# Performance work log

Hardware: AMD Instinct MI355X
Metric: run time of the kernel (lower is better)

## Reference

```python
import jax, jax.numpy as jnp
import numpy as np

L = 3; D = 128; H = 8; RBF = 16; SBF = 112
N = 60000; E = 300000; A = 8000; G = 256
EPS = 1e-8


def setup_inputs() -> dict:
    key = jax.random.key(0)
    ks = jax.random.split(key, 32)
    p = lambda i, shape: jax.random.normal(ks[i], shape, jnp.float32) * 0.05
    inp = {}
    inp['x'] = jax.random.normal(ks[0], (N, D), jnp.float32)
    inp['node_rbf'] = jax.random.uniform(ks[1], (N, RBF), jnp.float32)
    inp['edge_sbf'] = jax.random.uniform(ks[2], (E, SBF), jnp.float32)
    inp['edge_index'] = jax.random.randint(ks[3], (2, E), 0, N)
    inp['pair_atom_idx'] = jax.random.randint(ks[4], (E,), 0, A)
    inp['edge_index_0'] = jax.random.randint(ks[5], (N,), 0, A)
    inp['atom_batch'] = jnp.sort(jax.random.randint(ks[6], (A,), 0, G))
    inp['batch'] = jnp.sort(jax.random.randint(ks[7], (N,), 0, G))
    inp['edgenn_w1'] = p(8, (L, D, D)); inp['edgenn_b1'] = jnp.zeros((L, D))
    inp['edgenn_w2'] = p(9, (L, D, D)); inp['edgenn_b2'] = jnp.zeros((L, D))
    inp['conv_wq'] = p(10, (L, D, D)); inp['conv_wk'] = p(11, (L, D, D))
    inp['conv_wv'] = p(12, (L, D, D)); inp['conv_we'] = p(13, (L, D, D))
    inp['conv_wsbf'] = p(14, (L, SBF, D)); inp['conv_bsbf'] = jnp.zeros((L, D))
    inp['conv_wrbf'] = p(15, (L, RBF, D))
    inp['dense_w'] = p(16, (L, D, D)); inp['dense_b'] = jnp.zeros((L, D))
    inp['bf_w'] = p(17, (L, 2, D, D)); inp['bf_b'] = jnp.zeros((L, 2, D))
    inp['af_w'] = p(18, (L, 4, D, D)); inp['af_b'] = jnp.zeros((L, 4, D))
    inp['read_wrbf'] = p(19, (L + 1, RBF, D))
    inp['read_w1'] = p(20, (L + 1, D, D)); inp['read_b1'] = jnp.zeros((L + 1, D))
    inp['read_w2'] = p(21, (L + 1, D, D)); inp['read_b2'] = jnp.zeros((L + 1, D))
    inp['read_w3'] = p(22, (L + 1, D, 1)); inp['read_b3'] = jnp.zeros((L + 1, 1))
    return inp


def _forward(x, node_rbf, edge_sbf, edge_index, pair_atom_idx, edge_index_0,
             atom_batch, batch, edgenn_w1, edgenn_b1, edgenn_w2, edgenn_b2,
             conv_wq, conv_wk, conv_wv, conv_we, conv_wsbf, conv_bsbf, conv_wrbf,
             dense_w, dense_b, bf_w, bf_b, af_w, af_b,
             read_wrbf, read_w1, read_b1, read_w2, read_b2, read_w3, read_b3):
    segsum = jax.ops.segment_sum
    silu = jax.nn.silu
    src, dst = edge_index[0], edge_index[1]
    C = D // H

    def readout(i, h):
        # AtomWise: rbf-gated node features, scatter to atoms, small MLP -> [A,1]
        g = h * (node_rbf @ read_wrbf[i])
        atoms = segsum(g, edge_index_0, num_segments=A)
        a = silu(atoms @ read_w1[i] + read_b1[i])
        a = silu(a @ read_w2[i] + read_b2[i])
        return a @ read_w3[i] + read_b3[i]

    def res_block(h, w, b):
        # DimeNet-style ResidualLayer: x + act(lin2(act(lin1(x))))
        return h + silu(silu(h @ w[0] + b[0]) @ w[1] + b[1])

    def graph_norm(h):
        # batch-aware LayerNorm (graph mode, affine=False)
        cnt = segsum(jnp.ones((N,), h.dtype), batch, num_segments=G) * D
        mean = segsum(h.sum(-1), batch, num_segments=G) / cnt
        hc = h - mean[batch][:, None]
        var = segsum((hc * hc).sum(-1), batch, num_segments=G) / cnt
        return hc * jax.lax.rsqrt(var + EPS)[batch][:, None]

    out = x
    results = readout(0, out)
    for i in range(L):
        res0 = out
        atoms_rep = segsum(out, edge_index_0, num_segments=A)  # scatter_add to atoms
        ea = atoms_rep[pair_atom_idx]                           # gather per conv-edge
        ea = silu(ea @ edgenn_w1[i] + edgenn_b1[i]) @ edgenn_w2[i] + edgenn_b2[i]
        # SBFTransformerConv: TransformerConv with sbf-modulated messages + rbf gate
        q = (out @ conv_wq[i]).reshape(N, H, C)
        k = (out @ conv_wk[i]).reshape(N, H, C)
        v = (out @ conv_wv[i]).reshape(N, H, C)
        ek = (ea @ conv_we[i]).reshape(E, H, C)
        kj = k[src] + ek
        logit = (q[dst] * kj).sum(-1) / jnp.sqrt(jnp.asarray(C, out.dtype))  # [E,H]
        m = jax.ops.segment_max(logit, dst, num_segments=N)
        ex = jnp.exp(logit - m[dst])
        alpha = ex / (segsum(ex, dst, num_segments=N)[dst] + 1e-16)
        sw = (edge_sbf @ conv_wsbf[i] + conv_bsbf[i]).reshape(E, H, C)
        msg = (v[src] + ek) * alpha[:, :, None] * sw
        h = segsum(msg, dst, num_segments=N).reshape(N, D)
        out = h * (node_rbf @ conv_wrbf[i])
        out = graph_norm(out)
        out = res_block(out, bf_w[i], bf_b[i])
        out = silu(out @ dense_w[i] + dense_b[i])
        out = out + res0
        out = res_block(out, af_w[i, :2], af_b[i, :2])
        out = res_block(out, af_w[i, 2:], af_b[i, 2:])
        results = results + readout(i + 1, out)
    graphs = segsum(results, atom_batch, num_segments=G)  # [G,1]
    return graphs.reshape(-1) / L


def reference(x, node_rbf, edge_sbf, edge_index, pair_atom_idx, edge_index_0,
              atom_batch, batch, edgenn_w1, edgenn_b1, edgenn_w2, edgenn_b2,
              conv_wq, conv_wk, conv_wv, conv_we, conv_wsbf, conv_bsbf, conv_wrbf,
              dense_w, dense_b, bf_w, bf_b, af_w, af_b,
              read_wrbf, read_w1, read_b1, read_w2, read_b2, read_w3, read_b3):
    return _forward(x, node_rbf, edge_sbf, edge_index, pair_atom_idx, edge_index_0,
                    atom_batch, batch, edgenn_w1, edgenn_b1, edgenn_w2, edgenn_b2,
                    conv_wq, conv_wk, conv_wv, conv_we, conv_wsbf, conv_bsbf, conv_wrbf,
                    dense_w, dense_b, bf_w, bf_b, af_w, af_b,
                    read_wrbf, read_w1, read_b1, read_w2, read_b2, read_w3, read_b3)
```

## Files before the change

### kernel.cpp

```cpp
#include <hip/hip_runtime.h>
#include <math.h>

#define D    128
#define NH   8
#define RBFD 16
#define SBFD 112
#define LAYERS 3

typedef __attribute__((ext_vector_type(8))) short bf16x8;
typedef __attribute__((ext_vector_type(4))) float f32x4;

__device__ __forceinline__ float siluf(float x){ return x / (1.0f + __expf(-x)); }

__device__ __forceinline__ short f2bf(float f){
  union { float f; unsigned u; } v; v.f = f;
  unsigned r = v.u + 0x7FFFu + ((v.u >> 16) & 1u);
  return (short)(r >> 16);
}
__device__ __forceinline__ float bflo(unsigned u){ return __uint_as_float(u << 16); }
__device__ __forceinline__ float bfhi(unsigned u){ return __uint_as_float(u & 0xFFFF0000u); }

template<int DIN, int ACT, bool GATHER, bool HASB, bool HASRES, bool PERM, bool OUTBF>
__global__ __launch_bounds__(256, 2) void k_gemm(
    const float* __restrict__ X, const int* __restrict__ gidx,
    const float* __restrict__ W, const float* __restrict__ bias,
    const float* res, void* __restrict__ Yv, const int* __restrict__ operm, int M)
{
  __shared__ short Wt[128 * 128];
  if (DIN < 128){
    for (int i = threadIdx.x; i < 128 * 128; i += 256) Wt[i] = 0;
    __syncthreads();
  }
  for (int i = threadIdx.x; i < DIN * 128; i += 256){
    int k = i >> 7, c = i & 127;
    Wt[c * 128 + k] = f2bf(W[i]);
  }
  __syncthreads();

  const int lane = threadIdx.x & 63;
  const int wave = threadIdx.x >> 6;
  const int col0 = lane & 15;
  const int kg   = lane >> 4;

  bf16x8 Bf[8][4];
  #pragma unroll
  for (int ct = 0; ct < 8; ct++)
    #pragma unroll
    for (int s = 0; s < 4; s++)
      Bf[ct][s] = *(const bf16x8*)&Wt[(ct * 16 + col0) * 128 + s * 32 + kg * 8];

  float bs[8];
  if (HASB){
    #pragma unroll
    for (int ct = 0; ct < 8; ct++) bs[ct] = bias[ct * 16 + col0];
  }

  float* __restrict__ Yf = (float*)Yv;
  unsigned short* __restrict__ Yb = (unsigned short*)Yv;

  const long tiles = ((long)M + 63) >> 6;
  for (long t = blockIdx.x; t < tiles; t += gridDim.x){
    const long rbase = t * 64 + wave * 16;
    const long arow  = rbase + col0;
    long srow = 0;
    if (arow < M) srow = GATHER ? (long)gidx[arow] : arow;
    const float* Xp = X + srow * DIN;

    bf16x8 Af[4];
    #pragma unroll
    for (int s = 0; s < 4; s++){
      const int kb = s * 32 + kg * 8;
      bf16x8 a;
      if (DIN == 128 || kb + 8 <= DIN){
        float4 lo = *(const float4*)(Xp + kb);
        float4 hi = *(const float4*)(Xp + kb + 4);
        a[0]=f2bf(lo.x); a[1]=f2bf(lo.y); a[2]=f2bf(lo.z); a[3]=f2bf(lo.w);
        a[4]=f2bf(hi.x); a[5]=f2bf(hi.y); a[6]=f2bf(hi.z); a[7]=f2bf(hi.w);
      } else {
        #pragma unroll
        for (int j = 0; j < 8; j++) a[j] = 0;
      }
      Af[s] = a;
    }

    f32x4 acc[8];
    #pragma unroll
    for (int ct = 0; ct < 8; ct++){ acc[ct][0]=0.f; acc[ct][1]=0.f; acc[ct][2]=0.f; acc[ct][3]=0.f; }
    #pragma unroll
    for (int ct = 0; ct < 8; ct++)
      #pragma unroll
      for (int s = 0; s < 4; s++)
        acc[ct] = __builtin_amdgcn_mfma_f32_16x16x32_bf16(Af[s], Bf[ct][s], acc[ct], 0, 0, 0);

    #pragma unroll
    for (int r = 0; r < 4; r++){
      const long orow = rbase + kg * 4 + r;
      if (orow >= M) continue;
      const long wrow = PERM ? (long)operm[orow] : orow;
      #pragma unroll
      for (int ct = 0; ct < 8; ct++){
        const int c = ct * 16 + col0;
        float v = acc[ct][r];
        if (HASB) v += bs[ct];
        if (ACT)  v = siluf(v);
        if (HASRES) v += res[orow * D + c];
        if (OUTBF) Yb[wrow * D + c] = (unsigned short)f2bf(v);
        else       Yf[wrow * D + c] = v;
      }
    }
  }
}

__global__ __launch_bounds__(256, 2) void k_gemm2(
    const float* __restrict__ X, const int* __restrict__ gidx,
    const float* __restrict__ W1, const float* __restrict__ b1,
    const float* __restrict__ W2, const float* __restrict__ b2,
    unsigned short* __restrict__ Y, const int* __restrict__ operm, int M)
{
  __shared__ short W1t[128 * 128];
  __shared__ short W2t[128 * 128];
  __shared__ short Ts[64 * 128];
  for (int i = threadIdx.x; i < 128 * 128; i += 256){
    int k = i >> 7, c = i & 127;
    W1t[c * 128 + k] = f2bf(W1[i]);
    W2t[c * 128 + k] = f2bf(W2[i]);
  }
  __syncthreads();

  const int lane = threadIdx.x & 63;
  const int wave = threadIdx.x >> 6;
  const int col0 = lane & 15;
  const int kg   = lane >> 4;

  bf16x8 B1f[8][4];
  #pragma unroll
  for (int ct = 0; ct < 8; ct++)
    #pragma unroll
    for (int s = 0; s < 4; s++)
      B1f[ct][s] = *(const bf16x8*)&W1t[(ct * 16 + col0) * 128 + s * 32 + kg * 8];

  float bs1[8], bs2[8];
  #pragma unroll
  for (int ct = 0; ct < 8; ct++){ bs1[ct] = b1[ct * 16 + col0]; bs2[ct] = b2[ct * 16 + col0]; }

  const long tiles = ((long)M + 63) >> 6;
  for (long t = blockIdx.x; t < tiles; t += gridDim.x){
    const long rbase = t * 64 + wave * 16;
    const long arow  = rbase + col0;
    long srow = 0;
    if (arow < M) srow = (long)gidx[arow];
    const float* Xp = X + srow * D;

    bf16x8 Af[4];
    #pragma unroll
    for (int s = 0; s < 4; s++){
      const int kb = s * 32 + kg * 8;
      float4 lo = *(const float4*)(Xp + kb);
      float4 hi = *(const float4*)(Xp + kb + 4);
      bf16x8 a;
      a[0]=f2bf(lo.x); a[1]=f2bf(lo.y); a[2]=f2bf(lo.z); a[3]=f2bf(lo.w);
      a[4]=f2bf(hi.x); a[5]=f2bf(hi.y); a[6]=f2bf(hi.z); a[7]=f2bf(hi.w);
      Af[s] = a;
    }

    f32x4 acc[8];
    #pragma unroll
    for (int ct = 0; ct < 8; ct++){ acc[ct][0]=0.f; acc[ct][1]=0.f; acc[ct][2]=0.f; acc[ct][3]=0.f; }
    #pragma unroll
    for (int ct = 0; ct < 8; ct++)
      #pragma unroll
      for (int s = 0; s < 4; s++)
        acc[ct] = __builtin_amdgcn_mfma_f32_16x16x32_bf16(Af[s], B1f[ct][s], acc[ct], 0, 0, 0);

    #pragma unroll
    for (int ct = 0; ct < 8; ct++){
      const int c = ct * 16 + col0;
      #pragma unroll
      for (int r = 0; r < 4; r++){
        const int row = wave * 16 + kg * 4 + r;
        const int gg = (c >> 3) ^ (row & 7);
        Ts[row * 128 + gg * 8 + (c & 7)] = f2bf(siluf(acc[ct][r] + bs1[ct]));
      }
    }
    __syncthreads();

    const int row2 = wave * 16 + col0;
    bf16x8 A2f[4];
    #pragma unroll
    for (int s = 0; s < 4; s++){
      const int chunk = (s * 4 + kg) ^ (row2 & 7);
      A2f[s] = *(const bf16x8*)&Ts[row2 * 128 + chunk * 8];
    }
    __syncthreads();

    #pragma unroll
    for (int ct = 0; ct < 8; ct++){ acc[ct][0]=0.f; acc[ct][1]=0.f; acc[ct][2]=0.f; acc[ct][3]=0.f; }
    #pragma unroll
    for (int ct = 0; ct < 8; ct++){
      bf16x8 B2v[4];
      #pragma unroll
      for (int s = 0; s < 4; s++)
        B2v[s] = *(const bf16x8*)&W2t[(ct * 16 + col0) * 128 + s * 32 + kg * 8];
      #pragma unroll
      for (int s = 0; s < 4; s++)
        acc[ct] = __builtin_amdgcn_mfma_f32_16x16x32_bf16(A2f[s], B2v[s], acc[ct], 0, 0, 0);
    }

    #pragma unroll
    for (int r = 0; r < 4; r++){
      const long orow = rbase + kg * 4 + r;
      if (orow >= M) continue;
      const long wrow = (long)operm[orow];
      #pragma unroll
      for (int ct = 0; ct < 8; ct++){
        const int c = ct * 16 + col0;
        Y[wrow * D + c] = (unsigned short)f2bf(acc[ct][r] + bs2[ct]);
      }
    }
  }
}

template<bool NORM>
__global__ __launch_bounds__(256, 2) void k_res2(
    const float* __restrict__ X,
    const float* __restrict__ W1, const float* __restrict__ b1,
    const float* __restrict__ W2, const float* __restrict__ b2,
    const int* __restrict__ batch, const float* __restrict__ meanG,
    const float* __restrict__ rstdG, float* __restrict__ Y, int M)
{
  __shared__ short W1t[128 * 128];
  __shared__ short W2t[128 * 128];
  __shared__ short Ts[64 * 128];
  for (int i = threadIdx.x; i < 128 * 128; i += 256){
    int k = i >> 7, c = i & 127;
    W1t[c * 128 + k] = f2bf(W1[i]);
    W2t[c * 128 + k] = f2bf(W2[i]);
  }
  __syncthreads();

  const int lane = threadIdx.x & 63;
  const int wave = threadIdx.x >> 6;
  const int col0 = lane & 15;
  const int kg   = lane >> 4;

  bf16x8 B1f[8][4];
  #pragma unroll
  for (int ct = 0; ct < 8; ct++)
    #pragma unroll
    for (int s = 0; s < 4; s++)
      B1f[ct][s] = *(const bf16x8*)&W1t[(ct * 16 + col0) * 128 + s * 32 + kg * 8];

  float bs1[8], bs2[8];
  #pragma unroll
  for (int ct = 0; ct < 8; ct++){ bs1[ct] = b1[ct * 16 + col0]; bs2[ct] = b2[ct * 16 + col0]; }

  const long tiles = ((long)M + 63) >> 6;
  for (long t = blockIdx.x; t < tiles; t += gridDim.x){
    const long rbase = t * 64 + wave * 16;
    const long arow  = rbase + col0;
    const float* Xp = X + (arow < M ? arow : 0) * D;
    float xm = 0.f, xr = 1.f;
    if (NORM && arow < M){ int g = batch[arow]; xm = meanG[g]; xr = rstdG[g]; }

    bf16x8 Af[4];
    #pragma unroll
    for (int s = 0; s < 4; s++){
      const int kb = s * 32 + kg * 8;
      float4 lo = *(const float4*)(Xp + kb);
      float4 hi = *(const float4*)(Xp + kb + 4);
      bf16x8 a;
      a[0]=f2bf((lo.x-xm)*xr); a[1]=f2bf((lo.y-xm)*xr); a[2]=f2bf((lo.z-xm)*xr); a[3]=f2bf((lo.w-xm)*xr);
      a[4]=f2bf((hi.x-xm)*xr); a[5]=f2bf((hi.y-xm)*xr); a[6]=f2bf((hi.z-xm)*xr); a[7]=f2bf((hi.w-xm)*xr);
      Af[s] = a;
    }

    f32x4 acc[8];
    #pragma unroll
    for (int ct = 0; ct < 8; ct++){ acc[ct][0]=0.f; acc[ct][1]=0.f; acc[ct][2]=0.f; acc[ct][3]=0.f; }
    #pragma unroll
    for (int ct = 0; ct < 8; ct++)
      #pragma unroll
      for (int s = 0; s < 4; s++)
        acc[ct] = __builtin_amdgcn_mfma_f32_16x16x32_bf16(Af[s], B1f[ct][s], acc[ct], 0, 0, 0);

    #pragma unroll
    for (int ct = 0; ct < 8; ct++){
      const int c = ct * 16 + col0;
      #pragma unroll
      for (int r = 0; r < 4; r++){
        const int row = wave * 16 + kg * 4 + r;
        const int gg = (c >> 3) ^ (row & 7);
        Ts[row * 128 + gg * 8 + (c & 7)] = f2bf(siluf(acc[ct][r] + bs1[ct]));
      }
    }
    __syncthreads();

    const int row2 = wave * 16 + col0;
    bf16x8 A2f[4];
    #pragma unroll
    for (int s = 0; s < 4; s++){
      const int chunk = (s * 4 + kg) ^ (row2 & 7);
      A2f[s] = *(const bf16x8*)&Ts[row2 * 128 + chunk * 8];
    }
    __syncthreads();

    #pragma unroll
    for (int ct = 0; ct < 8; ct++){ acc[ct][0]=0.f; acc[ct][1]=0.f; acc[ct][2]=0.f; acc[ct][3]=0.f; }
    #pragma unroll
    for (int ct = 0; ct < 8; ct++){
      bf16x8 B2v[4];
      #pragma unroll
      for (int s = 0; s < 4; s++)
        B2v[s] = *(const bf16x8*)&W2t[(ct * 16 + col0) * 128 + s * 32 + kg * 8];
      #pragma unroll
      for (int s = 0; s < 4; s++)
        acc[ct] = __builtin_amdgcn_mfma_f32_16x16x32_bf16(A2f[s], B2v[s], acc[ct], 0, 0, 0);
    }

    #pragma unroll
    for (int r = 0; r < 4; r++){
      const long orow = rbase + kg * 4 + r;
      if (orow >= M) continue;
      float rm = 0.f, rr = 1.f;
      if (NORM){ int g = batch[orow]; rm = meanG[g]; rr = rstdG[g]; }
      #pragma unroll
      for (int ct = 0; ct < 8; ct++){
        const int c = ct * 16 + col0;
        float base = X[orow * D + c];
        if (NORM) base = (base - rm) * rr;
        Y[orow * D + c] = base + siluf(acc[ct][r] + bs2[ct]);
      }
    }
  }
}

__global__ __launch_bounds__(256, 2) void k_read2(
    const float* __restrict__ X,
    const float* __restrict__ W1, const float* __restrict__ b1,
    const float* __restrict__ W2, const float* __restrict__ b2,
    const float* __restrict__ w3, const float* __restrict__ b3,
    float* __restrict__ results, int M)
{
  __shared__ short W1t[128 * 128];
  __shared__ short W2t[128 * 128];
  __shared__ short Ts[64 * 128];
  for (int i = threadIdx.x; i < 128 * 128; i += 256){
    int k = i >> 7, c = i & 127;
    W1t[c * 128 + k] = f2bf(W1[i]);
    W2t[c * 128 + k] = f2bf(W2[i]);
  }
  __syncthreads();

  const int lane = threadIdx.x & 63;
  const int wave = threadIdx.x >> 6;
  const int col0 = lane & 15;
  const int kg   = lane >> 4;

  bf16x8 B1f[8][4];
  #pragma unroll
  for (int ct = 0; ct < 8; ct++)
    #pragma unroll
    for (int s = 0; s < 4; s++)
      B1f[ct][s] = *(const bf16x8*)&W1t[(ct * 16 + col0) * 128 + s * 32 + kg * 8];

  float bs1[8], bs2[8], w3v[8];
  #pragma unroll
  for (int ct = 0; ct < 8; ct++){
    bs1[ct] = b1[ct * 16 + col0];
    bs2[ct] = b2[ct * 16 + col0];
    w3v[ct] = w3[ct * 16 + col0];
  }
  const float b3v = b3[0];

  const long tiles = ((long)M + 63) >> 6;
  for (long t = blockIdx.x; t < tiles; t += gridDim.x){
    const long rbase = t * 64 + wave * 16;
    const long arow  = rbase + col0;
    const float* Xp = X + (arow < M ? arow : 0) * D;

    bf16x8 Af[4];
    #pragma unroll
    for (int s = 0; s < 4; s++){
      const int kb = s * 32 + kg * 8;
      float4 lo = *(const float4*)(Xp + kb);
      float4 hi = *(const float4*)(Xp + kb + 4);
      bf16x8 a;
      a[0]=f2bf(lo.x); a[1]=f2bf(lo.y); a[2]=f2bf(lo.z); a[3]=f2bf(lo.w);
      a[4]=f2bf(hi.x); a[5]=f2bf(hi.y); a[6]=f2bf(hi.z); a[7]=f2bf(hi.w);
      Af[s] = a;
    }

    f32x4 acc[8];
    #pragma unroll
    for (int ct = 0; ct < 8; ct++){ acc[ct][0]=0.f; acc[ct][1]=0.f; acc[ct][2]=0.f; acc[ct][3]=0.f; }
    #pragma unroll
    for (int ct = 0; ct < 8; ct++)
      #pragma unroll
      for (int s = 0; s < 4; s++)
        acc[ct] = __builtin_amdgcn_mfma_f32_16x16x32_bf16(Af[s], B1f[ct][s], acc[ct], 0, 0, 0);

    #pragma unroll
    for (int ct = 0; ct < 8; ct++){
      const int c = ct * 16 + col0;
      #pragma unroll
      for (int r = 0; r < 4; r++){
        const int row = wave * 16 + kg * 4 + r;
        const int gg = (c >> 3) ^ (row & 7);
        Ts[row * 128 + gg * 8 + (c & 7)] = f2bf(siluf(acc[ct][r] + bs1[ct]));
      }
    }
    __syncthreads();

    const int row2 = wave * 16 + col0;
    bf16x8 A2f[4];
    #pragma unroll
    for (int s = 0; s < 4; s++){
      const int chunk = (s * 4 + kg) ^ (row2 & 7);
      A2f[s] = *(const bf16x8*)&Ts[row2 * 128 + chunk * 8];
    }
    __syncthreads();

    #pragma unroll
    for (int ct = 0; ct < 8; ct++){ acc[ct][0]=0.f; acc[ct][1]=0.f; acc[ct][2]=0.f; acc[ct][3]=0.f; }
    #pragma unroll
    for (int ct = 0; ct < 8; ct++){
      bf16x8 B2v[4];
      #pragma unroll
      for (int s = 0; s < 4; s++)
        B2v[s] = *(const bf16x8*)&W2t[(ct * 16 + col0) * 128 + s * 32 + kg * 8];
      #pragma unroll
      for (int s = 0; s < 4; s++)
        acc[ct] = __builtin_amdgcn_mfma_f32_16x16x32_bf16(A2f[s], B2v[s], acc[ct], 0, 0, 0);
    }

    #pragma unroll
    for (int r = 0; r < 4; r++){
      float vr = 0.f;
      #pragma unroll
      for (int ct = 0; ct < 8; ct++)
        vr += siluf(acc[ct][r] + bs2[ct]) * w3v[ct];
      #pragma unroll
      for (int off = 1; off < 16; off <<= 1) vr += __shfl_xor(vr, off, 64);
      const long orow = rbase + kg * 4 + r;
      if (col0 == 0 && orow < M) results[orow] += vr + b3v;
    }
  }
}

__global__ void k_hist(const int* __restrict__ idx, int* __restrict__ cnt, int M)
{
  for (long i = (long)blockIdx.x * 256 + threadIdx.x; i < M; i += (long)gridDim.x * 256)
    atomicAdd(&cnt[idx[i]], 1);
}

__global__ void k_scan(const int* __restrict__ cnt, int* __restrict__ rowptr, int M)
{
  __shared__ int buf[1024];
  const int tid = threadIdx.x;
  const int PT = 16;
  int carry = 0;
  for (int base = 0; base < M; base += 1024 * PT){
    int loc[PT]; int s = 0;
    #pragma unroll
    for (int j = 0; j < PT; j++){
      int i = base + tid * PT + j;
      loc[j] = (i < M) ? cnt[i] : 0;
      s += loc[j];
    }
    buf[tid] = s; __syncthreads();
    for (int off = 1; off < 1024; off <<= 1){
      int t = (tid >= off) ? buf[tid - off] : 0;
      __syncthreads();
      buf[tid] += t;
      __syncthreads();
    }
    int run = buf[tid] - s + carry;
    carry += buf[1023];
    __syncthreads();
    #pragma unroll
    for (int j = 0; j < PT; j++){
      int i = base + tid * PT + j;
      if (i < M) rowptr[i] = run;
      run += loc[j];
    }
  }
  if (tid == 0) rowptr[M] = carry;
}

__global__ void k_fill(const int* __restrict__ idx, const int* __restrict__ rowptr,
                       int* __restrict__ cursor, int* __restrict__ ids, int M)
{
  for (long i = (long)blockIdx.x * 256 + threadIdx.x; i < M; i += (long)gridDim.x * 256){
    int sgm = idx[i];
    int pos = atomicAdd(&cursor[sgm], 1);
    ids[rowptr[sgm] + pos] = (int)i;
  }
}

__global__ void k_invsrc(const int* __restrict__ eids, const int* __restrict__ srcA,
                         int* __restrict__ invD, int* __restrict__ srcCSR, int E_)
{
  for (long i = (long)blockIdx.x * 256 + threadIdx.x; i < E_; i += (long)gridDim.x * 256){
    int e = eids[i];
    invD[e] = (int)i;
    srcCSR[i] = srcA[e];
  }
}

__global__ __launch_bounds__(256) void k_gather_sum(
    const float* __restrict__ X, const int* __restrict__ rowptr,
    const int* __restrict__ ids, float* __restrict__ Yat, int A_)
{
  const int lane = threadIdx.x & 63;
  const int wv   = threadIdx.x >> 6;
  for (long a = (long)blockIdx.x * 4 + wv; a < A_; a += (long)gridDim.x * 4){
    int beg = rowptr[a], end = rowptr[a + 1];
    float a0 = 0.f, a1 = 0.f;
    for (int i = beg; i < end; i++){
      const float* xp = X + (long)ids[i] * D;
      a0 += xp[lane]; a1 += xp[lane + 64];
    }
    Yat[a * D + lane] = a0; Yat[a * D + lane + 64] = a1;
  }
}

__global__ __launch_bounds__(256) void k_gather_gate_sum(
    const float* __restrict__ X, const float* __restrict__ rbf,
    const float* __restrict__ Wr, const int* __restrict__ rowptr,
    const int* __restrict__ ids, float* __restrict__ Yat, int A_)
{
  __shared__ float Wrs[RBFD * D];
  for (int i = threadIdx.x; i < RBFD * D; i += 256) Wrs[i] = Wr[i];
  __syncthreads();
  const int lane = threadIdx.x & 63;
  const int wv   = threadIdx.x >> 6;
  for (long a = (long)blockIdx.x * 4 + wv; a < A_; a += (long)gridDim.x * 4){
    int beg = rowptr[a], end = rowptr[a + 1];
    float a0 = 0.f, a1 = 0.f;
    for (int i = beg; i < end; i++){
      long n = ids[i];
      const float* xp = X + n * D;
      const float* rb = rbf + n * RBFD;
      float g0 = 0.f, g1 = 0.f;
      #pragma unroll
      for (int r = 0; r < RBFD; r++){
        float rv = rb[r];
        g0 += rv * Wrs[r * D + lane];
        g1 += rv * Wrs[r * D + lane + 64];
      }
      a0 += xp[lane] * g0; a1 += xp[lane + 64] * g1;
    }
    Yat[a * D + lane] = a0; Yat[a * D + lane + 64] = a1;
  }
}

__global__ __launch_bounds__(256) void k_attn(
    const unsigned short* __restrict__ q, const unsigned short* __restrict__ k,
    const unsigned short* __restrict__ v, const unsigned short* __restrict__ ek,
    const unsigned short* __restrict__ sw,
    const int* __restrict__ rowptr, const int* __restrict__ srcCSR,
    const float* __restrict__ rbf, const float* __restrict__ Wr,
    const int* __restrict__ batch,
    double* __restrict__ sums, double* __restrict__ sumsq,
    float* __restrict__ h, int Nn)
{
  __shared__ float Wrs[RBFD * D];
  for (int i = threadIdx.x; i < RBFD * D; i += 256) Wrs[i] = Wr[i];
  __syncthreads();
  const int lane = threadIdx.x & 63;
  const int wv   = threadIdx.x >> 6;
  for (long d = (long)blockIdx.x * 4 + wv; d < Nn; d += (long)gridDim.x * 4){
    const int beg = rowptr[d], end = rowptr[d + 1];
    const unsigned qp = *(const unsigned*)(q + d * D + 2 * lane);
    const float q0 = bflo(qp), q1 = bfhi(qp);
    float l = 0.f, a0 = 0.f, a1 = 0.f;
    for (int i = beg; i < end; i += 4){
      unsigned kk[4], vv[4], ee[4], ssw[4];
      #pragma unroll
      for (int j = 0; j < 4; j++){
        const long idx = (i + j < end) ? (long)(i + j) : (long)(end - 1);
        const long s = srcCSR[idx];
        kk[j]  = *(const unsigned*)(k  + s * D + 2 * lane);
        vv[j]  = *(const unsigned*)(v  + s * D + 2 * lane);
        ee[j]  = *(const unsigned*)(ek + idx * D + 2 * lane);
        ssw[j] = *(const unsigned*)(sw + idx * D + 2 * lane);
      }
      #pragma unroll
      for (int j = 0; j < 4; j++){
        const float valid = (i + j < end) ? 1.f : 0.f;
        float e0 = bflo(ee[j]), e1 = bfhi(ee[j]);
        float t = q0 * (bflo(kk[j]) + e0) + q1 * (bfhi(kk[j]) + e1);
        t += __shfl_xor(t, 1, 64);
        t += __shfl_xor(t, 2, 64);
        t += __shfl_xor(t, 4, 64);
        float w = __expf(t * 0.25f) * valid;
        float u0 = (bflo(vv[j]) + e0) * bflo(ssw[j]);
        float u1 = (bfhi(vv[j]) + e1) * bfhi(ssw[j]);
        l += w; a0 += w * u0; a1 += w * u1;
      }
    }
    const float inv = 1.f / (l + 1e-16f);
    a0 *= inv; a1 *= inv;
    const float* rb = rbf + d * RBFD;
    float g0 = 0.f, g1 = 0.f;
    #pragma unroll
    for (int r = 0; r < RBFD; r++){
      float rv = rb[r];
      g0 += rv * Wrs[r * D + 2 * lane];
      g1 += rv * Wrs[r * D + 2 * lane + 1];
    }
    a0 *= g0; a1 *= g1;
    *(float2*)(h + d * D + 2 * lane) = make_float2(a0, a1);
    float ss = a0 + a1, qq = a0 * a0 + a1 * a1;
    #pragma unroll
    for (int off = 1; off < 64; off <<= 1){
      ss += __shfl_xor(ss, off, 64);
      qq += __shfl_xor(qq, off, 64);
    }
    if (lane == 0){
      int g = batch[d];
      atomicAdd(&sums[g], (double)ss);
      atomicAdd(&sumsq[g], (double)qq);
    }
  }
}

__global__ void k_count(const int* __restrict__ batch, int* __restrict__ cnt, int M)
{
  for (long i = (long)blockIdx.x * 256 + threadIdx.x; i < M; i += (long)gridDim.x * 256)
    atomicAdd(&cnt[batch[i]], 1);
}

__global__ void k_norm_final(const double* __restrict__ sums, const double* __restrict__ sumsq,
                             const int* __restrict__ cnt, float* __restrict__ meanG,
                             float* __restrict__ rstdG)
{
  int g = threadIdx.x;
  double c = (double)cnt[g] * (double)D;
  double mean = sums[g] / c;
  double var = sumsq[g] / c - mean * mean;
  meanG[g] = (float)mean;
  rstdG[g] = (float)(1.0 / sqrt(var + 1e-8));
}

__global__ void k_final(const float* __restrict__ results, const int* __restrict__ ab,
                        float* __restrict__ out, int A_)
{
  int i = blockIdx.x * 256 + threadIdx.x;
  if (i < A_) atomicAdd(&out[ab[i]], results[i] / 3.0f);
}

__global__ void k_w2e(const float* __restrict__ w2, const float* __restrict__ we,
                      float* __restrict__ W2e)
{
  int i = blockIdx.x >> 7;
  int r = blockIdx.x & 127;
  int c = threadIdx.x;
  const float* w2p = w2 + (size_t)i * D * D + (size_t)r * D;
  const float* wep = we + (size_t)i * D * D;
  float acc = 0.f;
  for (int j = 0; j < D; j++) acc += w2p[j] * wep[j * D + c];
  W2e[(size_t)i * D * D + (size_t)r * D + c] = acc;
}

__global__ void k_b2e(const float* __restrict__ b2, const float* __restrict__ we,
                      float* __restrict__ B2e)
{
  int i = blockIdx.x; int c = threadIdx.x;
  float acc = 0.f;
  for (int j = 0; j < D; j++) acc += b2[(size_t)i * D + j] * we[(size_t)i * D * D + j * D + c];
  B2e[(size_t)i * D + c] = acc;
}

extern "C" void kernel_launch(void* const* d_in, const int* in_sizes, int n_in,
                              void* d_out, int out_size, void* d_ws, size_t ws_size,
                              hipStream_t stream)
{
  const float* x          = (const float*)d_in[0];
  const float* node_rbf   = (const float*)d_in[1];
  const float* edge_sbf   = (const float*)d_in[2];
  const int*   edge_index = (const int*)d_in[3];
  const int*   pair_idx   = (const int*)d_in[4];
  const int*   eidx0      = (const int*)d_in[5];
  const int*   atom_batch = (const int*)d_in[6];
  const int*   batch      = (const int*)d_in[7];
  const float* edgenn_w1  = (const float*)d_in[8];
  const float* edgenn_b1  = (const float*)d_in[9];
  const float* edgenn_w2  = (const float*)d_in[10];
  const float* edgenn_b2  = (const float*)d_in[11];
  const float* conv_wq    = (const float*)d_in[12];
  const float* conv_wk    = (const float*)d_in[13];
  const float* conv_wv    = (const float*)d_in[14];
  const float* conv_we    = (const float*)d_in[15];
  const float* conv_wsbf  = (const float*)d_in[16];
  const float* conv_bsbf  = (const float*)d_in[17];
  const float* conv_wrbf  = (const float*)d_in[18];
  const float* dense_w    = (const float*)d_in[19];
  const float* dense_b    = (const float*)d_in[20];
  const float* bf_w       = (const float*)d_in[21];
  const float* bf_b       = (const float*)d_in[22];
  const float* af_w       = (const float*)d_in[23];
  const float* af_b       = (const float*)d_in[24];
  const float* read_wrbf  = (const float*)d_in[25];
  const float* read_w1    = (const float*)d_in[26];
  const float* read_b1    = (const float*)d_in[27];
  const float* read_w2    = (const float*)d_in[28];
  const float* read_b2    = (const float*)d_in[29];
  const float* read_w3    = (const float*)d_in[30];
  const float* read_b3    = (const float*)d_in[31];

  const int N = in_sizes[0] / D;
  const int E = in_sizes[4];
  const int A = in_sizes[6];
  const int G = out_size;

  char* p = (char*)d_ws;
  auto carve = [&](size_t bytes)->char*{ char* r = p; p += (bytes + 255) & ~(size_t)255; return r; };
  unsigned short* ekb  = (unsigned short*)carve((size_t)E * D * 2);
  unsigned short* swb  = (unsigned short*)carve((size_t)E * D * 2);
  unsigned short* qb   = (unsigned short*)carve((size_t)N * D * 2);
  unsigned short* kb   = (unsigned short*)carve((size_t)N * D * 2);
  unsigned short* vb   = (unsigned short*)carve((size_t)N * D * 2);
  float*    hbuf    = (float*)carve((size_t)N * D * 4);
  float*    ping0   = (float*)carve((size_t)N * D * 4);
  float*    ping1   = (float*)carve((size_t)N * D * 4);
  float*    bufAtoms= (float*)carve((size_t)A * D * 4);
  float*    results = (float*)carve((size_t)A * 4);
  double*   sumG    = (double*)carve((size_t)G * 8);
  double*   sumsqG  = (double*)carve((size_t)G * 8);
  int*      cntG    = (int*)carve((size_t)G * 4);
  float*    meanG   = (float*)carve((size_t)G * 4);
  float*    rstdG   = (float*)carve((size_t)G * 4);
  float*    W2e     = (float*)carve((size_t)LAYERS * D * D * 4);
  float*    B2e     = (float*)carve((size_t)LAYERS * D * 4);
  int*      rowptrD = (int*)carve((size_t)(N + 1) * 4);
  int*      eidsD   = (int*)carve((size_t)E * 4);
  int*      invD    = (int*)carve((size_t)E * 4);
  int*      srcCSR  = (int*)carve((size_t)E * 4);
  int*      cntD    = (int*)carve((size_t)N * 4);
  int*      rowptrA = (int*)carve((size_t)(A + 1) * 4);
  int*      idsA    = (int*)carve((size_t)N * 4);
  int*      cntA    = (int*)carve((size_t)A * 4);

  const int* srcA = edge_index;
  const int* dstA = edge_index + E;

  auto ew_grid = [](long total){ long b = (total + 255) / 256; return (int)(b < 4096 ? b : 4096); };
  auto gemm_grid = [](int M){ long t = ((long)M + 63) / 64; return (int)(t < 1024 ? t : 1024); };
  const int gridAttn = (N + 3) / 4;
  const int gridAtom = (A + 3) / 4;

  hipMemsetAsync(cntG, 0, (size_t)G * 4, stream);
  hipMemsetAsync(results, 0, (size_t)A * 4, stream);
  hipMemsetAsync(d_out, 0, (size_t)G * 4, stream);
  k_count<<<ew_grid(N), 256, 0, stream>>>(batch, cntG, N);
  k_w2e<<<LAYERS * D, D, 0, stream>>>(edgenn_w2, conv_we, W2e);
  k_b2e<<<LAYERS, D, 0, stream>>>(edgenn_b2, conv_we, B2e);
  hipMemsetAsync(cntD, 0, (size_t)N * 4, stream);
  k_hist<<<ew_grid(E), 256, 0, stream>>>(dstA, cntD, E);
  k_scan<<<1, 1024, 0, stream>>>(cntD, rowptrD, N);
  hipMemsetAsync(cntD, 0, (size_t)N * 4, stream);
  k_fill<<<ew_grid(E), 256, 0, stream>>>(dstA, rowptrD, cntD, eidsD, E);
  k_invsrc<<<ew_grid(E), 256, 0, stream>>>(eidsD, srcA, invD, srcCSR, E);
  hipMemsetAsync(cntA, 0, (size_t)A * 4, stream);
  k_hist<<<ew_grid(N), 256, 0, stream>>>(eidx0, cntA, N);
  k_scan<<<1, 1024, 0, stream>>>(cntA, rowptrA, A);
  hipMemsetAsync(cntA, 0, (size_t)A * 4, stream);
  k_fill<<<ew_grid(N), 256, 0, stream>>>(eidx0, rowptrA, cntA, idsA, N);

  auto readout = [&](int i, const float* hb){
    k_gather_gate_sum<<<gridAtom, 256, 0, stream>>>(hb, node_rbf, read_wrbf + (size_t)i * RBFD * D,
                                                    rowptrA, idsA, bufAtoms, A);
    k_read2<<<gemm_grid(A), 256, 0, stream>>>(bufAtoms,
        read_w1 + (size_t)i*D*D, read_b1 + (size_t)i*D,
        read_w2 + (size_t)i*D*D, read_b2 + (size_t)i*D,
        read_w3 + (size_t)i*D, read_b3 + i, results, A);
  };

  readout(0, x);

  const float* cur = x;
  float* pp[2] = {ping0, ping1};
  for (int i = 0; i < LAYERS; i++){
    float* nxt = pp[i & 1];
    const size_t oDD = (size_t)i * D * D;
    k_gather_sum<<<gridAtom, 256, 0, stream>>>(cur, rowptrA, idsA, bufAtoms, A);
    k_gemm2<<<gemm_grid(E),256,0,stream>>>(bufAtoms, pair_idx, edgenn_w1 + oDD, edgenn_b1 + (size_t)i*D,
                                           W2e + oDD, B2e + (size_t)i*D, ekb, invD, E);
    k_gemm<D,0,false,false,false,false,true><<<gemm_grid(N),256,0,stream>>>(cur, nullptr, conv_wq + oDD, nullptr, nullptr, qb, nullptr, N);
    k_gemm<D,0,false,false,false,false,true><<<gemm_grid(N),256,0,stream>>>(cur, nullptr, conv_wk + oDD, nullptr, nullptr, kb, nullptr, N);
    k_gemm<D,0,false,false,false,false,true><<<gemm_grid(N),256,0,stream>>>(cur, nullptr, conv_wv + oDD, nullptr, nullptr, vb, nullptr, N);
    k_gemm<SBFD,0,false,true,false,true,true><<<gemm_grid(E),256,0,stream>>>(edge_sbf, nullptr, conv_wsbf + (size_t)i*SBFD*D, conv_bsbf + (size_t)i*D, nullptr, swb, invD, E);
    hipMemsetAsync(sumG, 0, (size_t)G * 16, stream);
    k_attn<<<gridAttn, 256, 0, stream>>>(qb, kb, vb, ekb, swb, rowptrD, srcCSR,
                                         node_rbf, conv_wrbf + (size_t)i*RBFD*D, batch,
                                         sumG, sumsqG, hbuf, N);
    k_norm_final<<<1, G, 0, stream>>>(sumG, sumsqG, cntG, meanG, rstdG);
    k_res2<true><<<gemm_grid(N),256,0,stream>>>(hbuf, bf_w + (size_t)i*2*D*D, bf_b + (size_t)i*2*D,
                                                bf_w + (size_t)i*2*D*D + D*D, bf_b + (size_t)i*2*D + D,
                                                batch, meanG, rstdG, hbuf, N);
    k_gemm<D,1,false,true,true,false,false><<<gemm_grid(N),256,0,stream>>>(hbuf, nullptr, dense_w + oDD, dense_b + (size_t)i*D, cur, nxt, nullptr, N);
    k_res2<false><<<gemm_grid(N),256,0,stream>>>(nxt, af_w + (size_t)i*4*D*D,         af_b + (size_t)i*4*D,
                                                 af_w + (size_t)i*4*D*D + D*D,       af_b + (size_t)i*4*D + D,
                                                 nullptr, nullptr, nullptr, nxt, N);
    k_res2<false><<<gemm_grid(N),256,0,stream>>>(nxt, af_w + (size_t)i*4*D*D + 2*D*D, af_b + (size_t)i*4*D + 2*D,
                                                 af_w + (size_t)i*4*D*D + 3*D*D,     af_b + (size_t)i*4*D + 3*D,
                                                 nullptr, nullptr, nullptr, nxt, N);
    readout(i + 1, nxt);
    cur = nxt;
  }
  k_final<<<(A + 255) / 256, 256, 0, stream>>>(results, atom_batch, (float*)d_out, A);
}
```

Before: 3.132 ms.

## Split attention into per-edge score kernel and CSR aggregation; pre-convert SBF to bf16

The fused per-destination attention kernel is split in two. A new edge-parallel kernel computes per-head exp scores and the gated value message once per edge, with wide 16-byte loads, and writes them to scratch buffers. A lighter CSR aggregation kernel then sums the weighted messages per destination. Separately, edge_sbf is converted to bf16 once at setup so the three per-layer SBF GEMMs read half the bytes. The cost is an extra E×D bf16 write and read plus a weight buffer each layer, in exchange for more parallel, coalesced edge work and less gather work inside the aggregation loop.

Result: no change. 3.191 ms (+1.9%).

```diff
diff --git a/kernel.cpp b/kernel.cpp
--- a/kernel.cpp
+++ b/kernel.cpp
@@ -20,9 +20,9 @@
 __device__ __forceinline__ float bflo(unsigned u){ return __uint_as_float(u << 16); }
 __device__ __forceinline__ float bfhi(unsigned u){ return __uint_as_float(u & 0xFFFF0000u); }
 
-template<int DIN, int ACT, bool GATHER, bool HASB, bool HASRES, bool PERM, bool OUTBF>
+template<int DIN, int ACT, bool GATHER, bool HASB, bool HASRES, bool PERM, bool OUTBF, bool INBF>
 __global__ __launch_bounds__(256, 2) void k_gemm(
-    const float* __restrict__ X, const int* __restrict__ gidx,
+    const void* __restrict__ Xv, const int* __restrict__ gidx,
     const float* __restrict__ W, const float* __restrict__ bias,
     const float* res, void* __restrict__ Yv, const int* __restrict__ operm, int M)
 {
@@ -55,6 +55,8 @@
     for (int ct = 0; ct < 8; ct++) bs[ct] = bias[ct * 16 + col0];
   }
 
+  const float* __restrict__ Xf = (const float*)Xv;
+  const unsigned short* __restrict__ Xb = (const unsigned short*)Xv;
   float* __restrict__ Yf = (float*)Yv;
   unsigned short* __restrict__ Yb = (unsigned short*)Yv;
 
@@ -64,7 +66,6 @@
     const long arow  = rbase + col0;
     long srow = 0;
     if (arow < M) srow = GATHER ? (long)gidx[arow] : arow;
-    const float* Xp = X + srow * DIN;
 
     bf16x8 Af[4];
     #pragma unroll
@@ -72,10 +73,15 @@
       const int kb = s * 32 + kg * 8;
       bf16x8 a;
       if (DIN == 128 || kb + 8 <= DIN){
-        float4 lo = *(const float4*)(Xp + kb);
-        float4 hi = *(const float4*)(Xp + kb + 4);
-        a[0]=f2bf(lo.x); a[1]=f2bf(lo.y); a[2]=f2bf(lo.z); a[3]=f2bf(lo.w);
-        a[4]=f2bf(hi.x); a[5]=f2bf(hi.y); a[6]=f2bf(hi.z); a[7]=f2bf(hi.w);
+        if (INBF){
+          a = *(const bf16x8*)(Xb + srow * DIN + kb);
+        } else {
+          const float* Xp = Xf + srow * DIN;
+          float4 lo = *(const float4*)(Xp + kb);
+          float4 hi = *(const float4*)(Xp + kb + 4);
+          a[0]=f2bf(lo.x); a[1]=f2bf(lo.y); a[2]=f2bf(lo.z); a[3]=f2bf(lo.w);
+          a[4]=f2bf(hi.x); a[5]=f2bf(hi.y); a[6]=f2bf(hi.z); a[7]=f2bf(hi.w);
+        }
       } else {
         #pragma unroll
         for (int j = 0; j < 8; j++) a[j] = 0;
@@ -498,12 +504,26 @@
 }
 
 __global__ void k_invsrc(const int* __restrict__ eids, const int* __restrict__ srcA,
-                         int* __restrict__ invD, int* __restrict__ srcCSR, int E_)
+                         const int* __restrict__ dstA,
+                         int* __restrict__ invD, int* __restrict__ srcCSR,
+                         int* __restrict__ dstCSR, int E_)
 {
   for (long i = (long)blockIdx.x * 256 + threadIdx.x; i < E_; i += (long)gridDim.x * 256){
     int e = eids[i];
     invD[e] = (int)i;
     srcCSR[i] = srcA[e];
+    dstCSR[i] = dstA[e];
+  }
+}
+
+__global__ void k_cvt(const float* __restrict__ X, unsigned short* __restrict__ Y, long total4)
+{
+  for (long i = (long)blockIdx.x * 256 + threadIdx.x; i < total4; i += (long)gridDim.x * 256){
+    float4 xv = *(const float4*)(X + i * 4);
+    ushort4 o;
+    o.x = (unsigned short)f2bf(xv.x); o.y = (unsigned short)f2bf(xv.y);
+    o.z = (unsigned short)f2bf(xv.z); o.w = (unsigned short)f2bf(xv.w);
+    *(ushort4*)(Y + i * 4) = o;
   }
 }
 
@@ -554,11 +574,49 @@
   }
 }
 
-__global__ __launch_bounds__(256) void k_attn(
+__global__ __launch_bounds__(256) void k_edge(
     const unsigned short* __restrict__ q, const unsigned short* __restrict__ k,
     const unsigned short* __restrict__ v, const unsigned short* __restrict__ ek,
     const unsigned short* __restrict__ sw,
-    const int* __restrict__ rowptr, const int* __restrict__ srcCSR,
+    const int* __restrict__ srcCSR, const int* __restrict__ dstCSR,
+    unsigned short* __restrict__ ve, float* __restrict__ w, int E_)
+{
+  const long tid = (long)blockIdx.x * 256 + threadIdx.x;
+  const long i = tid >> 4;
+  if (i >= E_) return;
+  const int ll = (int)(threadIdx.x & 15);
+  const int co = ll * 8;
+  const long s = srcCSR[i], d = dstCSR[i];
+  uint4 ekv = *(const uint4*)(ek + i * D + co);
+  uint4 swv = *(const uint4*)(sw + i * D + co);
+  uint4 kv  = *(const uint4*)(k + s * D + co);
+  uint4 vv  = *(const uint4*)(v + s * D + co);
+  uint4 qv  = *(const uint4*)(q + d * D + co);
+  const unsigned* ep = (const unsigned*)&ekv;
+  const unsigned* sp = (const unsigned*)&swv;
+  const unsigned* kp = (const unsigned*)&kv;
+  const unsigned* vp = (const unsigned*)&vv;
+  const unsigned* qp = (const unsigned*)&qv;
+  float t = 0.f;
+  unsigned out[4];
+  #pragma unroll
+  for (int j = 0; j < 4; j++){
+    float e0 = bflo(ep[j]), e1 = bfhi(ep[j]);
+    t += bflo(qp[j]) * (bflo(kp[j]) + e0) + bfhi(qp[j]) * (bfhi(kp[j]) + e1);
+    float u0 = (bflo(vp[j]) + e0) * bflo(sp[j]);
+    float u1 = (bfhi(vp[j]) + e1) * bfhi(sp[j]);
+    unsigned lo16 = (unsigned)(unsigned short)f2bf(u0);
+    unsigned hi16 = (unsigned)(unsigned short)f2bf(u1);
+    out[j] = lo16 | (hi16 << 16);
+  }
+  t += __shfl_xor(t, 1, 64);
+  if ((ll & 1) == 0) w[i * NH + (ll >> 1)] = __expf(t * 0.25f);
+  *(uint4*)(ve + i * D + co) = make_uint4(out[0], out[1], out[2], out[3]);
+}
+
+__global__ __launch_bounds__(256) void k_attn2(
+    const unsigned short* __restrict__ ve, const float* __restrict__ w,
+    const int* __restrict__ rowptr,
     const float* __restrict__ rbf, const float* __restrict__ Wr,
     const int* __restrict__ batch,
     double* __restrict__ sums, double* __restrict__ sumsq,
@@ -569,34 +627,23 @@
   __syncthreads();
   const int lane = threadIdx.x & 63;
   const int wv   = threadIdx.x >> 6;
+  const int h8   = lane >> 3;
   for (long d = (long)blockIdx.x * 4 + wv; d < Nn; d += (long)gridDim.x * 4){
     const int beg = rowptr[d], end = rowptr[d + 1];
-    const unsigned qp = *(const unsigned*)(q + d * D + 2 * lane);
-    const float q0 = bflo(qp), q1 = bfhi(qp);
     float l = 0.f, a0 = 0.f, a1 = 0.f;
     for (int i = beg; i < end; i += 4){
-      unsigned kk[4], vv[4], ee[4], ssw[4];
+      unsigned vv[4]; float ww[4];
       #pragma unroll
       for (int j = 0; j < 4; j++){
         const long idx = (i + j < end) ? (long)(i + j) : (long)(end - 1);
-        const long s = srcCSR[idx];
-        kk[j]  = *(const unsigned*)(k  + s * D + 2 * lane);
-        vv[j]  = *(const unsigned*)(v  + s * D + 2 * lane);
-        ee[j]  = *(const unsigned*)(ek + idx * D + 2 * lane);
-        ssw[j] = *(const unsigned*)(sw + idx * D + 2 * lane);
+        vv[j] = *(const unsigned*)(ve + idx * D + 2 * lane);
+        ww[j] = (i + j < end) ? w[idx * NH + h8] : 0.f;
       }
       #pragma unroll
       for (int j = 0; j < 4; j++){
-        const float valid = (i + j < end) ? 1.f : 0.f;
-        float e0 = bflo(ee[j]), e1 = bfhi(ee[j]);
-        float t = q0 * (bflo(kk[j]) + e0) + q1 * (bfhi(kk[j]) + e1);
-        t += __shfl_xor(t, 1, 64);
-        t += __shfl_xor(t, 2, 64);
-        t += __shfl_xor(t, 4, 64);
-        float w = __expf(t * 0.25f) * valid;
-        float u0 = (bflo(vv[j]) + e0) * bflo(ssw[j]);
-        float u1 = (bfhi(vv[j]) + e1) * bfhi(ssw[j]);
-        l += w; a0 += w * u0; a1 += w * u1;
+        l  += ww[j];
+        a0 += ww[j] * bflo(vv[j]);
+        a1 += ww[j] * bfhi(vv[j]);
       }
     }
     const float inv = 1.f / (l + 1e-16f);
@@ -718,9 +765,12 @@
   auto carve = [&](size_t bytes)->char*{ char* r = p; p += (bytes + 255) & ~(size_t)255; return r; };
   unsigned short* ekb  = (unsigned short*)carve((size_t)E * D * 2);
   unsigned short* swb  = (unsigned short*)carve((size_t)E * D * 2);
+  unsigned short* veb  = (unsigned short*)carve((size_t)E * D * 2);
   unsigned short* qb   = (unsigned short*)carve((size_t)N * D * 2);
   unsigned short* kb   = (unsigned short*)carve((size_t)N * D * 2);
   unsigned short* vb   = (unsigned short*)carve((size_t)N * D * 2);
+  unsigned short* sbfb = (unsigned short*)carve((size_t)E * SBFD * 2);
+  float*    wbuf    = (float*)carve((size_t)E * NH * 4);
   float*    hbuf    = (float*)carve((size_t)N * D * 4);
   float*    ping0   = (float*)carve((size_t)N * D * 4);
   float*    ping1   = (float*)carve((size_t)N * D * 4);
@@ -737,6 +787,7 @@
   int*      eidsD   = (int*)carve((size_t)E * 4);
   int*      invD    = (int*)carve((size_t)E * 4);
   int*      srcCSR  = (int*)carve((size_t)E * 4);
+  int*      dstCSR  = (int*)carve((size_t)E * 4);
   int*      cntD    = (int*)carve((size_t)N * 4);
   int*      rowptrA = (int*)carve((size_t)(A + 1) * 4);
   int*      idsA    = (int*)carve((size_t)N * 4);
@@ -749,6 +800,7 @@
   auto gemm_grid = [](int M){ long t = ((long)M + 63) / 64; return (int)(t < 1024 ? t : 1024); };
   const int gridAttn = (N + 3) / 4;
   const int gridAtom = (A + 3) / 4;
+  const int gridEdge = (int)(((long)E * 16 + 255) / 256);
 
   hipMemsetAsync(cntG, 0, (size_t)G * 4, stream);
   hipMemsetAsync(results, 0, (size_t)A * 4, stream);
@@ -756,12 +808,13 @@
   k_count<<<ew_grid(N), 256, 0, stream>>>(batch, cntG, N);
   k_w2e<<<LAYERS * D, D, 0, stream>>>(edgenn_w2, conv_we, W2e);
   k_b2e<<<LAYERS, D, 0, stream>>>(edgenn_b2, conv_we, B2e);
+  k_cvt<<<4096, 256, 0, stream>>>(edge_sbf, sbfb, ((long)E * SBFD) / 4);
   hipMemsetAsync(cntD, 0, (size_t)N * 4, stream);
   k_hist<<<ew_grid(E), 256, 0, stream>>>(dstA, cntD, E);
   k_scan<<<1, 1024, 0, stream>>>(cntD, rowptrD, N);
   hipMemsetAsync(cntD, 0, (size_t)N * 4, stream);
   k_fill<<<ew_grid(E), 256, 0, stream>>>(dstA, rowptrD, cntD, eidsD, E);
-  k_invsrc<<<ew_grid(E), 256, 0, stream>>>(eidsD, srcA, invD, srcCSR, E);
+  k_invsrc<<<ew_grid(E), 256, 0, stream>>>(eidsD, srcA, dstA, invD, srcCSR, dstCSR, E);
   hipMemsetAsync(cntA, 0, (size_t)A * 4, stream);
   k_hist<<<ew_grid(N), 256, 0, stream>>>(eidx0, cntA, N);
   k_scan<<<1, 1024, 0, stream>>>(cntA, rowptrA, A);
@@ -787,19 +840,20 @@
     k_gather_sum<<<gridAtom, 256, 0, stream>>>(cur, rowptrA, idsA, bufAtoms, A);
     k_gemm2<<<gemm_grid(E),256,0,stream>>>(bufAtoms, pair_idx, edgenn_w1 + oDD, edgenn_b1 + (size_t)i*D,
                                            W2e + oDD, B2e + (size_t)i*D, ekb, invD, E);
-    k_gemm<D,0,false,false,false,false,true><<<gemm_grid(N),256,0,stream>>>(cur, nullptr, conv_wq + oDD, nullptr, nullptr, qb, nullptr, N);
-    k_gemm<D,0,false,false,false,false,true><<<gemm_grid(N),256,0,stream>>>(cur, nullptr, conv_wk + oDD, nullptr, nullptr, kb, nullptr, N);
-    k_gemm<D,0,false,false,false,false,true><<<gemm_grid(N),256,0,stream>>>(cur, nullptr, conv_wv + oDD, nullptr, nullptr, vb, nullptr, N);
-    k_gemm<SBFD,0,false,true,false,true,true><<<gemm_grid(E),256,0,stream>>>(edge_sbf, nullptr, conv_wsbf + (size_t)i*SBFD*D, conv_bsbf + (size_t)i*D, nullptr, swb, invD, E);
+    k_gemm<D,0,false,false,false,false,true,false><<<gemm_grid(N),256,0,stream>>>(cur, nullptr, conv_wq + oDD, nullptr, nullptr, qb, nullptr, N);
+    k_gemm<D,0,false,false,false,false,true,false><<<gemm_grid(N),256,0,stream>>>(cur, nullptr, conv_wk + oDD, nullptr, nullptr, kb, nullptr, N);
+    k_gemm<D,0,false,false,false,false,true,false><<<gemm_grid(N),256,0,stream>>>(cur, nullptr, conv_wv + oDD, nullptr, nullptr, vb, nullptr, N);
+    k_gemm<SBFD,0,false,true,false,true,true,true><<<gemm_grid(E),256,0,stream>>>(sbfb, nullptr, conv_wsbf + (size_t)i*SBFD*D, conv_bsbf + (size_t)i*D, nullptr, swb, invD, E);
+    k_edge<<<gridEdge, 256, 0, stream>>>(qb, kb, vb, ekb, swb, srcCSR, dstCSR, veb, wbuf, E);
     hipMemsetAsync(sumG, 0, (size_t)G * 16, stream);
-    k_attn<<<gridAttn, 256, 0, stream>>>(qb, kb, vb, ekb, swb, rowptrD, srcCSR,
-                                         node_rbf, conv_wrbf + (size_t)i*RBFD*D, batch,
-                                         sumG, sumsqG, hbuf, N);
+    k_attn2<<<gridAttn, 256, 0, stream>>>(veb, wbuf, rowptrD,
+                                          node_rbf, conv_wrbf + (size_t)i*RBFD*D, batch,
+                                          sumG, sumsqG, hbuf, N);
     k_norm_final<<<1, G, 0, stream>>>(sumG, sumsqG, cntG, meanG, rstdG);
     k_res2<true><<<gemm_grid(N),256,0,stream>>>(hbuf, bf_w + (size_t)i*2*D*D, bf_b + (size_t)i*2*D,
                                                 bf_w + (size_t)i*2*D*D + D*D, bf_b + (size_t)i*2*D + D,
                                                 batch, meanG, rstdG, hbuf, N);
-    k_gemm<D,1,false,true,true,false,false><<<gemm_grid(N),256,0,stream>>>(hbuf, nullptr, dense_w + oDD, dense_b + (size_t)i*D, cur, nxt, nullptr, N);
+    k_gemm<D,1,false,true,true,false,false,false><<<gemm_grid(N),256,0,stream>>>(hbuf, nullptr, dense_w + oDD, dense_b + (size_t)i*D, cur, nxt, nullptr, N);
     k_res2<false><<<gemm_grid(N),256,0,stream>>>(nxt, af_w + (size_t)i*4*D*D,         af_b + (size_t)i*4*D,
                                                  af_w + (size_t)i*4*D*D + D*D,       af_b + (size_t)i*4*D + D,
                                                  nullptr, nullptr, nullptr, nxt, N);
```
